# Kernel optimization log

Hardware: AMD Instinct MI355X
Metric: run time of the kernel (lower is better)

Reference implementation:

```python
import jax, jax.numpy as jnp
import numpy as np

B, T, I, H, L, O = 256, 256, 64, 2048, 4, 1

def setup_inputs() -> dict:
    key = jax.random.key(0)
    ks = jax.random.split(key, 8)
    # layer 0: input_size -> hidden (xavier-uniform-like scale)
    W_ih0 = jax.random.normal(ks[0], (H, I), jnp.float32) * (1.0 / np.sqrt(I))
    b_ih0 = jnp.zeros((H,), jnp.float32)
    # layers 1..L-1: hidden -> hidden, stacked
    W_ih_rest = jax.random.normal(ks[1], (L - 1, H, H), jnp.float32) * (1.0 / np.sqrt(H))
    b_ih_rest = jnp.zeros((L - 1, H), jnp.float32)
    # recurrent weights for all layers (orthogonal init approximated by scaled normal)
    W_hh = jax.random.normal(ks[2], (L, H, H), jnp.float32) * (1.0 / np.sqrt(H))
    # final fc
    W_fc = jax.random.normal(ks[3], (O, H), jnp.float32) * (1.0 / np.sqrt(H))
    b_fc = jnp.zeros((O,), jnp.float32)
    x = jax.random.normal(ks[4], (B, T, I), jnp.float32)
    return {"x": x, "W_ih0": W_ih0, "b_ih0": b_ih0, "W_ih_rest": W_ih_rest,
            "b_ih_rest": b_ih_rest, "W_hh": W_hh, "W_fc": W_fc, "b_fc": b_fc}

def reference(x, W_ih0, b_ih0, W_ih_rest, b_ih_rest, W_hh, W_fc, b_fc):
    # h_t^l = tanh(W_ih^l @ inp + b_ih^l + W_hh^l @ h_{t-1}^l); dropout_rate=0 (identity)
    h0 = jnp.zeros((L, B, H), x.dtype)
    xs = jnp.swapaxes(x, 0, 1)  # [T, B, I]

    def step(h, x_t):
        inp = x_t
        new_h = []
        for l in range(L):
            if l == 0:
                pre = inp @ W_ih0.T + b_ih0 + h[l] @ W_hh[l].T
            else:
                pre = inp @ W_ih_rest[l - 1].T + b_ih_rest[l - 1] + h[l] @ W_hh[l].T
            hl = jnp.tanh(pre)
            new_h.append(hl)
            inp = hl
        return jnp.stack(new_h, 0), None

    h_final, _ = jax.lax.scan(step, h0, xs)
    return h_final[-1] @ W_fc.T + b_fc  # [B, O]
```

## Files before the change

### kernel.cpp

```cpp
#include <hip/hip_runtime.h>
#include <hip/hip_bf16.h>


typedef unsigned short u16;
typedef __attribute__((ext_vector_type(8))) short short8;
typedef __attribute__((ext_vector_type(4))) float f32x4;

#define T_N 256
#define I_N 64
#define H_N 2048
#define L_N 4

static constexpr size_t S0_ELE = 2048ull * 2112ull;
static constexpr size_t SL_ELE = 2048ull * 4096ull;
static constexpr size_t WT_ELEMS = S0_ELE + 3ull * SL_ELE;
static constexpr size_t XS_ELEMS = 256ull * 256ull * 64ull;
static constexpr size_t HSLOT    = 256ull * 2048ull;
static constexpr size_t H_ELEMS  = 2ull * 4ull * HSLOT;

__device__ __forceinline__ u16 f2bf(float v) {
  __hip_bfloat16 b = __float2bfloat16(v);
  u16 u; __builtin_memcpy(&u, &b, 2); return u;
}
__device__ __forceinline__ float bf2f(u16 u) {
  __hip_bfloat16 b; __builtin_memcpy(&b, &u, 2);
  return __bfloat162float(b);
}

__device__ __forceinline__ void gl2lds16(const u16* g, u16* l) {
  __builtin_amdgcn_global_load_lds(
      (const __attribute__((address_space(1))) unsigned int*)g,
      (__attribute__((address_space(3))) unsigned int*)l, 16, 0, 0);
}

__global__ void prep_w(const float* __restrict__ W_ih0, const float* __restrict__ W_ih_rest,
                       const float* __restrict__ W_hh,
                       u16* __restrict__ wt_hi, u16* __restrict__ wt_lo) {
  const unsigned TOT = (unsigned)WT_ELEMS;
  for (unsigned i = blockIdx.x * 256u + threadIdx.x; i < TOT; i += gridDim.x * 256u) {
    int l, K, Kin; unsigned r;
    if (i < (unsigned)S0_ELE) { l = 0; r = i; K = 2112; Kin = 64; }
    else {
      unsigned j = i - (unsigned)S0_ELE;
      l = 1 + (int)(j / (unsigned)SL_ELE);
      r = j % (unsigned)SL_ELE; K = 4096; Kin = 2048;
    }
    unsigned n = r / (unsigned)K, k = r % (unsigned)K;
    float v;
    if ((int)k < Kin)
      v = (l == 0) ? W_ih0[(size_t)n * 64 + k]
                   : W_ih_rest[(((size_t)(l - 1)) * 2048 + n) * 2048 + k];
    else
      v = W_hh[(((size_t)l) * 2048 + n) * 2048 + (k - (unsigned)Kin)];
    u16 hi = f2bf(v);
    wt_hi[i] = hi;
    wt_lo[i] = f2bf(v - bf2f(hi));
  }
}

__global__ void prep_x(const float* __restrict__ x, u16* __restrict__ xs_hi, u16* __restrict__ xs_lo) {
  for (unsigned i = blockIdx.x * 256u + threadIdx.x; i < (unsigned)XS_ELEMS; i += gridDim.x * 256u) {
    float v = x[i];
    u16 hi = f2bf(v);
    xs_hi[i] = hi;
    xs_lo[i] = f2bf(v - bf2f(hi));
  }
}

__launch_bounds__(256, 2)
__global__ void phase_k(const u16* __restrict__ wt_hi, const u16* __restrict__ wt_lo,
                        const u16* __restrict__ xs_hi, const u16* __restrict__ xs_lo,
                        u16* __restrict__ h_hi, u16* __restrict__ h_lo,
                        const float* __restrict__ b_ih0, const float* __restrict__ b_ih_rest,
                        int s) {
  int bid = blockIdx.x;
  int xcd = bid & 7, slot = bid >> 3;
  int tm  = slot & 3;
  int tnl = (slot >> 2) & 3;
  int l   = slot >> 4;
  int tn  = xcd * 4 + tnl;
  int t   = s - l;
  if (t < 0 || t >= T_N) return;

  const int Kl  = (l == 0) ? 2112 : 4096;
  const size_t woff = (l == 0) ? 0ull : (S0_ELE + (size_t)(l - 1) * SL_ELE);
  const u16* wl_hi = wt_hi + woff;
  const u16* wl_lo = wt_lo + woff;

  const size_t ho_out  = ((size_t)((t & 1) * 4 + l)) * HSLOT;
  const size_t ho_self = ((size_t)(((t - 1) & 1) * 4 + l)) * HSLOT;
  const int lprev = (l > 0) ? (l - 1) : 0;
  const size_t ho_prevL = ((size_t)((t & 1) * 4 + lprev)) * HSLOT;

  __shared__ __align__(16) u16 Ahi[2][64 * 64];
  __shared__ __align__(16) u16 Alo[2][64 * 64];
  __shared__ __align__(16) u16 Bhi[2][64 * 64];
  __shared__ __align__(16) u16 Blo[2][64 * 64];

  const int tid = threadIdx.x;
  const int lane = tid & 63;
  const int l15 = lane & 15, g16 = lane >> 4;
  const int wid = tid >> 6;
  const int wave_m = (wid & 1) * 32, wave_n = (wid >> 1) * 32;

  f32x4 acc[2][2];
#pragma unroll
  for (int mi = 0; mi < 2; ++mi)
#pragma unroll
    for (int ni = 0; ni < 2; ++ni)
      acc[mi][ni] = (f32x4){0.f, 0.f, 0.f, 0.f};

  const int selfc0 = (l == 0) ? 1 : 32;
  const int kin    = (l == 0) ? 64 : 2048;

  auto issue_chunk = [&](int kc, int buf) {
#pragma unroll
    for (int it = 0; it < 2; ++it) {
      int G = it * 256 + tid;
      int r = G >> 3, gl = G & 7;
      int kg = (kc << 6) + ((gl ^ (r & 7)) << 3);
      int b = tm * 64 + r;
      const u16 *ph, *pl; size_t o;
      if (kc < selfc0) {
        if (l == 0) { o = ((size_t)b * T_N + t) * I_N + kg; ph = xs_hi; pl = xs_lo; }
        else        { o = ho_prevL + (size_t)b * H_N + kg;  ph = h_hi;  pl = h_lo; }
      } else {
        o = ho_self + (size_t)b * H_N + (kg - kin); ph = h_hi; pl = h_lo;
      }
      u16* dh = &Ahi[buf][(it * 256 + wid * 64) * 8];
      u16* dl = &Alo[buf][(it * 256 + wid * 64) * 8];
      gl2lds16(ph + o, dh);
      gl2lds16(pl + o, dl);
    }
#pragma unroll
    for (int it = 0; it < 2; ++it) {
      int G = it * 256 + tid;
      int r = G >> 3, gl = G & 7;
      size_t o = (size_t)(tn * 64 + r) * Kl + (kc << 6) + ((gl ^ (r & 7)) << 3);
      u16* dh = &Bhi[buf][(it * 256 + wid * 64) * 8];
      u16* dl = &Blo[buf][(it * 256 + wid * 64) * 8];
      gl2lds16(wl_hi + o, dh);
      gl2lds16(wl_lo + o, dl);
    }
  };

  const int nchunks = Kl >> 6;
  issue_chunk(0, 0);
  for (int kc = 0; kc < nchunks; ++kc) {
    const int cur = kc & 1;
    __syncthreads();
    if (kc + 1 < nchunks) issue_chunk(kc + 1, cur ^ 1);

#pragma unroll
    for (int ks = 0; ks < 2; ++ks) {
      const int glb = (ks << 2) + g16;
      short8 ah[2], al[2], bh[2], bl[2];
#pragma unroll
      for (int mi = 0; mi < 2; ++mi) {
        int r = wave_m + mi * 16 + l15;
        int idx = r * 64 + ((glb ^ (r & 7)) << 3);
        ah[mi] = *(const short8*)&Ahi[cur][idx];
        al[mi] = *(const short8*)&Alo[cur][idx];
      }
#pragma unroll
      for (int ni = 0; ni < 2; ++ni) {
        int r = wave_n + ni * 16 + l15;
        int idx = r * 64 + ((glb ^ (r & 7)) << 3);
        bh[ni] = *(const short8*)&Bhi[cur][idx];
        bl[ni] = *(const short8*)&Blo[cur][idx];
      }
#pragma unroll
      for (int mi = 0; mi < 2; ++mi)
#pragma unroll
        for (int ni = 0; ni < 2; ++ni) {
          acc[mi][ni] = __builtin_amdgcn_mfma_f32_16x16x32_bf16(ah[mi], bh[ni], acc[mi][ni], 0, 0, 0);
          acc[mi][ni] = __builtin_amdgcn_mfma_f32_16x16x32_bf16(ah[mi], bl[ni], acc[mi][ni], 0, 0, 0);
          acc[mi][ni] = __builtin_amdgcn_mfma_f32_16x16x32_bf16(al[mi], bh[ni], acc[mi][ni], 0, 0, 0);
        }
    }
  }

  const float* bias = (l == 0) ? b_ih0 : (b_ih_rest + (size_t)(l - 1) * H_N);
#pragma unroll
  for (int mi = 0; mi < 2; ++mi)
#pragma unroll
    for (int ni = 0; ni < 2; ++ni)
#pragma unroll
      for (int rg = 0; rg < 4; ++rg) {
        int bg = tm * 64 + wave_m + mi * 16 + g16 * 4 + rg;
        int ng = tn * 64 + wave_n + ni * 16 + l15;
        float v = acc[mi][ni][rg] + bias[ng];
        v = tanhf(v);
        u16 hi = f2bf(v);
        size_t o = ho_out + (size_t)bg * H_N + ng;
        h_hi[o] = hi;
        h_lo[o] = f2bf(v - bf2f(hi));
      }
}

__global__ void fc_k(const u16* __restrict__ h_hi, const u16* __restrict__ h_lo,
                     const float* __restrict__ W_fc, const float* __restrict__ b_fc,
                     float* __restrict__ out) {
  int b = blockIdx.x, tid = threadIdx.x;
  size_t base = ((size_t)(((T_N - 1) & 1) * 4 + 3)) * HSLOT + (size_t)b * H_N;
  float s = 0.f;
  for (int j = tid; j < H_N; j += 256)
    s += (bf2f(h_hi[base + j]) + bf2f(h_lo[base + j])) * W_fc[j];
  __shared__ float red[256];
  red[tid] = s; __syncthreads();
  for (int w = 128; w > 0; w >>= 1) {
    if (tid < w) red[tid] += red[tid + w];
    __syncthreads();
  }
  if (tid == 0) out[b] = red[0] + b_fc[0];
}

extern "C" void kernel_launch(void* const* d_in, const int* in_sizes, int n_in,
                              void* d_out, int out_size, void* d_ws, size_t ws_size,
                              hipStream_t stream) {
  const float* x         = (const float*)d_in[0];
  const float* W_ih0     = (const float*)d_in[1];
  const float* b_ih0     = (const float*)d_in[2];
  const float* W_ih_rest = (const float*)d_in[3];
  const float* b_ih_rest = (const float*)d_in[4];
  const float* W_hh      = (const float*)d_in[5];
  const float* W_fc      = (const float*)d_in[6];
  const float* b_fc      = (const float*)d_in[7];
  float* out = (float*)d_out;

  char* p = (char*)d_ws;
  auto carve = [&](size_t bytes) {
    char* q = p; p += (bytes + 255) & ~(size_t)255; return q;
  };
  u16* wt_hi = (u16*)carve(WT_ELEMS * 2);
  u16* wt_lo = (u16*)carve(WT_ELEMS * 2);
  u16* xs_hi = (u16*)carve(XS_ELEMS * 2);
  u16* xs_lo = (u16*)carve(XS_ELEMS * 2);
  u16* h_hi  = (u16*)carve(H_ELEMS * 2);
  u16* h_lo  = (u16*)carve(H_ELEMS * 2);

  hipMemsetAsync(h_hi, 0, H_ELEMS * 2 * 2, stream);
  prep_w<<<4096, 256, 0, stream>>>(W_ih0, W_ih_rest, W_hh, wt_hi, wt_lo);
  prep_x<<<2048, 256, 0, stream>>>(x, xs_hi, xs_lo);

  for (int s = 0; s < T_N + L_N - 1; ++s)
    phase_k<<<512, 256, 0, stream>>>(wt_hi, wt_lo, xs_hi, xs_lo, h_hi, h_lo,
                                     b_ih0, b_ih_rest, s);

  fc_k<<<256, 256, 0, stream>>>(h_hi, h_lo, W_fc, b_fc, out);
}
```

Measured before the change: 16.59 ms.

## Use 128x64 tiles with 512-thread blocks and load A fragments directly from global

Each block now covers a 128-row batch tile by 64 columns with 8 waves, halving the grid to 256 blocks. The activation (A) operand is no longer staged through LDS; each wave reads its MFMA fragments straight from global memory, and only the weight (B) tile is double-buffered in LDS, now with a 128-wide K chunk. Layer 0's packed K is padded from 2112 to 2176 with zeros so it divides into 128-wide chunks. This aims to cut weight refetch traffic and LDS pressure per step, at the cost of uncoalesced, unpipelined global loads for A and fewer, larger blocks.

```diff
diff --git a/kernel.cpp b/kernel.cpp
--- a/kernel.cpp
+++ b/kernel.cpp
@@ -10,9 +10,10 @@
 #define I_N 64
 #define H_N 2048
 #define L_N 4
-
-static constexpr size_t S0_ELE = 2048ull * 2112ull;
-static constexpr size_t SL_ELE = 2048ull * 4096ull;
+#define S0K 2176
+
+static constexpr size_t S0_ELE   = 2048ull * (size_t)S0K;
+static constexpr size_t SL_ELE   = 2048ull * 4096ull;
 static constexpr size_t WT_ELEMS = S0_ELE + 3ull * SL_ELE;
 static constexpr size_t XS_ELEMS = 256ull * 256ull * 64ull;
 static constexpr size_t HSLOT    = 256ull * 2048ull;
@@ -38,20 +39,21 @@
                        u16* __restrict__ wt_hi, u16* __restrict__ wt_lo) {
   const unsigned TOT = (unsigned)WT_ELEMS;
   for (unsigned i = blockIdx.x * 256u + threadIdx.x; i < TOT; i += gridDim.x * 256u) {
-    int l, K, Kin; unsigned r;
-    if (i < (unsigned)S0_ELE) { l = 0; r = i; K = 2112; Kin = 64; }
-    else {
+    float v;
+    if (i < (unsigned)S0_ELE) {
+      unsigned n = i / (unsigned)S0K, k = i % (unsigned)S0K;
+      if (k < 64u)         v = W_ih0[(size_t)n * 64 + k];
+      else if (k < 2112u)  v = W_hh[(size_t)n * 2048 + (k - 64u)];
+      else                 v = 0.f;
+    } else {
       unsigned j = i - (unsigned)S0_ELE;
-      l = 1 + (int)(j / (unsigned)SL_ELE);
-      r = j % (unsigned)SL_ELE; K = 4096; Kin = 2048;
-    }
-    unsigned n = r / (unsigned)K, k = r % (unsigned)K;
-    float v;
-    if ((int)k < Kin)
-      v = (l == 0) ? W_ih0[(size_t)n * 64 + k]
-                   : W_ih_rest[(((size_t)(l - 1)) * 2048 + n) * 2048 + k];
-    else
-      v = W_hh[(((size_t)l) * 2048 + n) * 2048 + (k - (unsigned)Kin)];
+      unsigned l = 1 + j / (unsigned)SL_ELE;
+      unsigned r = j % (unsigned)SL_ELE;
+      unsigned n = r / 4096u, k = r % 4096u;
+      v = (k < 2048u)
+            ? W_ih_rest[(((size_t)(l - 1)) * 2048 + n) * 2048 + k]
+            : W_hh[(((size_t)l) * 2048 + n) * 2048 + (k - 2048u)];
+    }
     u16 hi = f2bf(v);
     wt_hi[i] = hi;
     wt_lo[i] = f2bf(v - bf2f(hi));
@@ -67,7 +69,7 @@
   }
 }
 
-__launch_bounds__(256, 2)
+__launch_bounds__(512, 1)
 __global__ void phase_k(const u16* __restrict__ wt_hi, const u16* __restrict__ wt_lo,
                         const u16* __restrict__ xs_hi, const u16* __restrict__ xs_lo,
                         u16* __restrict__ h_hi, u16* __restrict__ h_lo,
@@ -75,14 +77,13 @@
                         int s) {
   int bid = blockIdx.x;
   int xcd = bid & 7, slot = bid >> 3;
-  int tm  = slot & 3;
-  int tnl = (slot >> 2) & 3;
-  int l   = slot >> 4;
-  int tn  = xcd * 4 + tnl;
+  int tm  = slot & 1;
+  int tn  = (xcd << 2) | ((slot >> 1) & 3);
+  int l   = slot >> 3;
   int t   = s - l;
   if (t < 0 || t >= T_N) return;
 
-  const int Kl  = (l == 0) ? 2112 : 4096;
+  const int Kl = (l == 0) ? S0K : 4096;
   const size_t woff = (l == 0) ? 0ull : (S0_ELE + (size_t)(l - 1) * SL_ELE);
   const u16* wl_hi = wt_hi + woff;
   const u16* wl_lo = wt_lo + woff;
@@ -92,16 +93,14 @@
   const int lprev = (l > 0) ? (l - 1) : 0;
   const size_t ho_prevL = ((size_t)((t & 1) * 4 + lprev)) * HSLOT;
 
-  __shared__ __align__(16) u16 Ahi[2][64 * 64];
-  __shared__ __align__(16) u16 Alo[2][64 * 64];
-  __shared__ __align__(16) u16 Bhi[2][64 * 64];
-  __shared__ __align__(16) u16 Blo[2][64 * 64];
+  __shared__ __align__(16) u16 Bhi[2][64 * 128];
+  __shared__ __align__(16) u16 Blo[2][64 * 128];
 
   const int tid = threadIdx.x;
   const int lane = tid & 63;
   const int l15 = lane & 15, g16 = lane >> 4;
   const int wid = tid >> 6;
-  const int wave_m = (wid & 1) * 32, wave_n = (wid >> 1) * 32;
+  const int wave_m = (wid & 3) * 32, wave_n = (wid >> 2) * 32;
 
   f32x4 acc[2][2];
 #pragma unroll
@@ -110,62 +109,56 @@
     for (int ni = 0; ni < 2; ++ni)
       acc[mi][ni] = (f32x4){0.f, 0.f, 0.f, 0.f};
 
-  const int selfc0 = (l == 0) ? 1 : 32;
-  const int kin    = (l == 0) ? 64 : 2048;
-
-  auto issue_chunk = [&](int kc, int buf) {
+  auto stage_B = [&](int kc, int buf) {
 #pragma unroll
     for (int it = 0; it < 2; ++it) {
-      int G = it * 256 + tid;
-      int r = G >> 3, gl = G & 7;
-      int kg = (kc << 6) + ((gl ^ (r & 7)) << 3);
-      int b = tm * 64 + r;
-      const u16 *ph, *pl; size_t o;
-      if (kc < selfc0) {
-        if (l == 0) { o = ((size_t)b * T_N + t) * I_N + kg; ph = xs_hi; pl = xs_lo; }
-        else        { o = ho_prevL + (size_t)b * H_N + kg;  ph = h_hi;  pl = h_lo; }
-      } else {
-        o = ho_self + (size_t)b * H_N + (kg - kin); ph = h_hi; pl = h_lo;
-      }
-      u16* dh = &Ahi[buf][(it * 256 + wid * 64) * 8];
-      u16* dl = &Alo[buf][(it * 256 + wid * 64) * 8];
-      gl2lds16(ph + o, dh);
-      gl2lds16(pl + o, dl);
-    }
-#pragma unroll
-    for (int it = 0; it < 2; ++it) {
-      int G = it * 256 + tid;
-      int r = G >> 3, gl = G & 7;
-      size_t o = (size_t)(tn * 64 + r) * Kl + (kc << 6) + ((gl ^ (r & 7)) << 3);
-      u16* dh = &Bhi[buf][(it * 256 + wid * 64) * 8];
-      u16* dl = &Blo[buf][(it * 256 + wid * 64) * 8];
+      int lin = (wid * 2 + it) * 64 + lane;
+      int r = lin >> 4, gsw = lin & 15;
+      size_t o = (size_t)(tn * 64 + r) * Kl + ((size_t)kc << 7) + (size_t)((gsw ^ (r & 7)) << 3);
+      u16* dh = &Bhi[buf][(wid * 2 + it) * 512];
+      u16* dl = &Blo[buf][(wid * 2 + it) * 512];
       gl2lds16(wl_hi + o, dh);
       gl2lds16(wl_lo + o, dl);
     }
   };
 
-  const int nchunks = Kl >> 6;
-  issue_chunk(0, 0);
-  for (int kc = 0; kc < nchunks; ++kc) {
+  const int nch = Kl >> 7;
+  stage_B(0, 0);
+  for (int kc = 0; kc < nch; ++kc) {
     const int cur = kc & 1;
     __syncthreads();
-    if (kc + 1 < nchunks) issue_chunk(kc + 1, cur ^ 1);
-
-#pragma unroll
-    for (int ks = 0; ks < 2; ++ks) {
-      const int glb = (ks << 2) + g16;
-      short8 ah[2], al[2], bh[2], bl[2];
+    if (kc + 1 < nch) stage_B(kc + 1, cur ^ 1);
+
+    short8 aH[4][2], aL[4][2];
+#pragma unroll
+    for (int ks = 0; ks < 4; ++ks) {
+      const int k = (kc << 7) + ks * 32;
+      const u16 *ph, *pl; size_t base; int xrow = 0;
+      if (l == 0) {
+        if (k < 64) { ph = xs_hi; pl = xs_lo; base = (size_t)k; xrow = 1; }
+        else        { ph = h_hi + ho_self; pl = h_lo + ho_self; base = (size_t)(k - 64); }
+      } else {
+        if (k < 2048) { ph = h_hi + ho_prevL; pl = h_lo + ho_prevL; base = (size_t)k; }
+        else          { ph = h_hi + ho_self;  pl = h_lo + ho_self;  base = (size_t)(k - 2048); }
+      }
 #pragma unroll
       for (int mi = 0; mi < 2; ++mi) {
-        int r = wave_m + mi * 16 + l15;
-        int idx = r * 64 + ((glb ^ (r & 7)) << 3);
-        ah[mi] = *(const short8*)&Ahi[cur][idx];
-        al[mi] = *(const short8*)&Alo[cur][idx];
-      }
+        int row = tm * 128 + wave_m + mi * 16 + l15;
+        size_t o = xrow ? (((size_t)row * T_N + t) * I_N + base + (size_t)(g16 * 8))
+                        : ((size_t)row * H_N + base + (size_t)(g16 * 8));
+        aH[ks][mi] = *(const short8*)(ph + o);
+        aL[ks][mi] = *(const short8*)(pl + o);
+      }
+    }
+
+#pragma unroll
+    for (int ks = 0; ks < 4; ++ks) {
+      short8 bh[2], bl[2];
 #pragma unroll
       for (int ni = 0; ni < 2; ++ni) {
         int r = wave_n + ni * 16 + l15;
-        int idx = r * 64 + ((glb ^ (r & 7)) << 3);
+        int gpos = (ks * 4 + g16) ^ (r & 7);
+        int idx = r * 128 + gpos * 8;
         bh[ni] = *(const short8*)&Bhi[cur][idx];
         bl[ni] = *(const short8*)&Blo[cur][idx];
       }
@@ -173,9 +166,9 @@
       for (int mi = 0; mi < 2; ++mi)
 #pragma unroll
         for (int ni = 0; ni < 2; ++ni) {
-          acc[mi][ni] = __builtin_amdgcn_mfma_f32_16x16x32_bf16(ah[mi], bh[ni], acc[mi][ni], 0, 0, 0);
-          acc[mi][ni] = __builtin_amdgcn_mfma_f32_16x16x32_bf16(ah[mi], bl[ni], acc[mi][ni], 0, 0, 0);
-          acc[mi][ni] = __builtin_amdgcn_mfma_f32_16x16x32_bf16(al[mi], bh[ni], acc[mi][ni], 0, 0, 0);
+          acc[mi][ni] = __builtin_amdgcn_mfma_f32_16x16x32_bf16(aH[ks][mi], bh[ni], acc[mi][ni], 0, 0, 0);
+          acc[mi][ni] = __builtin_amdgcn_mfma_f32_16x16x32_bf16(aH[ks][mi], bl[ni], acc[mi][ni], 0, 0, 0);
+          acc[mi][ni] = __builtin_amdgcn_mfma_f32_16x16x32_bf16(aL[ks][mi], bh[ni], acc[mi][ni], 0, 0, 0);
         }
     }
   }
@@ -187,7 +180,7 @@
     for (int ni = 0; ni < 2; ++ni)
 #pragma unroll
       for (int rg = 0; rg < 4; ++rg) {
-        int bg = tm * 64 + wave_m + mi * 16 + g16 * 4 + rg;
+        int bg = tm * 128 + wave_m + mi * 16 + g16 * 4 + rg;
         int ng = tn * 64 + wave_n + ni * 16 + l15;
         float v = acc[mi][ni][rg] + bias[ng];
         v = tanhf(v);
@@ -244,7 +237,7 @@
   prep_x<<<2048, 256, 0, stream>>>(x, xs_hi, xs_lo);
 
   for (int s = 0; s < T_N + L_N - 1; ++s)
-    phase_k<<<512, 256, 0, stream>>>(wt_hi, wt_lo, xs_hi, xs_lo, h_hi, h_lo,
+    phase_k<<<256, 512, 0, stream>>>(wt_hi, wt_lo, xs_hi, xs_lo, h_hi, h_lo,
                                      b_ih0, b_ih_rest, s);
 
   fc_k<<<256, 256, 0, stream>>>(h_hi, h_lo, W_fc, b_fc, out);
```

New measurement: 36.40 ms. +119.4%, slower.
